# Performance work log

Hardware: AMD Instinct MI355X
Metric: run time of the kernel (lower is better)

## Reference

```python
import jax, jax.numpy as jnp
import numpy as np

B, S, D, H, HID = 8, 1024, 768, 12, 3072
HD = D // H
EPS = 1e-5


def layernorm(x, g, b):
    mu = jnp.mean(x, axis=-1, keepdims=True)
    var = jnp.mean(jnp.square(x - mu), axis=-1, keepdims=True)
    return (x - mu) * jax.lax.rsqrt(var + EPS) * g + b


def setup_inputs() -> dict:
    key = jax.random.key(0)
    ks = jax.random.split(key, 8)
    s_d = 1.0 / np.sqrt(D)
    s_h = 1.0 / np.sqrt(HID)
    return {
        "x": jax.random.normal(ks[0], (B, S, D), jnp.float32),
        # attention projections (stored as [in, out])
        "wq": jax.random.normal(ks[1], (D, D), jnp.float32) * s_d,
        "bq": jnp.zeros((D,), jnp.float32),
        "wk": jax.random.normal(ks[2], (D, D), jnp.float32) * s_d,
        "bk": jnp.zeros((D,), jnp.float32),
        "wv": jax.random.normal(ks[3], (D, D), jnp.float32) * s_d,
        "bv": jnp.zeros((D,), jnp.float32),
        # layernorms
        "ln1_g": jnp.ones((D,), jnp.float32),
        "ln1_b": jnp.zeros((D,), jnp.float32),
        "ln2_g": jnp.ones((D,), jnp.float32),
        "ln2_b": jnp.zeros((D,), jnp.float32),
        # MLP
        "w_in": jax.random.normal(ks[4], (D, HID), jnp.float32) * s_d,
        "b_in": jnp.zeros((HID,), jnp.float32),
        "w_out": jax.random.normal(ks[5], (HID, D), jnp.float32) * s_h,
        "b_out": jnp.zeros((D,), jnp.float32),
    }


def reference(x, wq, bq, wk, bk, wv, bv, ln1_g, ln1_b, ln2_g, ln2_b,
              w_in, b_in, w_out, b_out):
    scale = HD ** -0.5
    # --- MHSA (note: original forward never applies out_proj) ---
    q = (x @ wq + bq).reshape(B, S, H, HD).transpose(0, 2, 1, 3)  # [B,H,S,hd]
    k = (x @ wk + bk).reshape(B, S, H, HD).transpose(0, 2, 1, 3)
    v = (x @ wv + bv).reshape(B, S, H, HD).transpose(0, 2, 1, 3)
    scores = jnp.einsum("bhqd,bhkd->bhqk", q, k)  # full NxN, as in source
    attn = jax.nn.softmax(scores * scale, axis=-1)
    ctx = jnp.einsum("bhqk,bhkd->bhqd", attn, v)
    ctx = ctx.transpose(0, 2, 1, 3).reshape(B, S, D)
    # --- residual: pre_ln applied to attention OUTPUT (as in source) ---
    x = x + layernorm(ctx, ln1_g, ln1_b)
    # --- MLP: GELU after BOTH linears (as in source), dropout=0 ---
    h = jax.nn.gelu(layernorm(x, ln2_g, ln2_b) @ w_in + b_in, approximate=False)
    h = jax.nn.gelu(h @ w_out + b_out, approximate=False)
    return x + h
```

## Files before the change

### kernel.cpp

```cpp
#include <hip/hip_runtime.h>
#include <math.h>

typedef __attribute__((ext_vector_type(8))) short short8;
typedef __attribute__((ext_vector_type(4))) short short4v;
typedef __attribute__((ext_vector_type(4))) float f32x4;

#define MFMA16(a, b, c) __builtin_amdgcn_mfma_f32_16x16x32_bf16(a, b, c, 0, 0, 0)

__device__ __forceinline__ short f2bf(float f) {
    union { float f; unsigned u; } v; v.f = f;
    unsigned r = v.u + 0x7fffu + ((v.u >> 16) & 1u);
    return (short)(r >> 16);
}
__device__ __forceinline__ float bf2f(short s) {
    union { unsigned u; float f; } v; v.u = ((unsigned)(unsigned short)s) << 16;
    return v.f;
}
__device__ __forceinline__ float gelu(float v) {
    float u = v * (1.0f + 0.044715f * v * v);
    float e = exp2f(-2.3021184f * u);
    return v * __builtin_amdgcn_rcpf(1.0f + e);
}
__device__ __forceinline__ float max3f(float a, float b, float c) {
    float d; asm("v_max3_f32 %0, %1, %2, %3" : "=v"(d) : "v"(a), "v"(b), "v"(c)); return d;
}
__device__ __forceinline__ void async16(const short* g, short* l) {
    __builtin_amdgcn_global_load_lds((const __attribute__((address_space(1))) void*)g,
                                     (__attribute__((address_space(3))) void*)l, 16, 0, 0);
}

__device__ __forceinline__ short8 build_pfrag(int lg, float x0, float x1, float x2, float x3,
                                              float x4, float x5, float x6, float x7) {
    unsigned a0, a1, b0, b1;
    asm("v_cvt_pk_bf16_f32 %0, %1, %2" : "=v"(a0) : "v"(x0), "v"(x1));
    asm("v_cvt_pk_bf16_f32 %0, %1, %2" : "=v"(a1) : "v"(x2), "v"(x3));
    asm("v_cvt_pk_bf16_f32 %0, %1, %2" : "=v"(b0) : "v"(x4), "v"(x5));
    asm("v_cvt_pk_bf16_f32 %0, %1, %2" : "=v"(b1) : "v"(x6), "v"(x7));
    unsigned u0 = (lg < 2) ? b0 : a0, u1 = (lg < 2) ? b1 : a1;
    unsigned v0 = (unsigned)__shfl_xor((int)u0, 32), v1 = (unsigned)__shfl_xor((int)u1, 32);
    unsigned w0 = (lg < 2) ? a0 : b0, w1 = (lg < 2) ? a1 : b1;
    bool sw = ((lg ^ (lg >> 1)) & 1) != 0;
    unsigned s0 = sw ? w0 : v0, s1 = sw ? w1 : v1;
    unsigned r0 = (unsigned)__shfl_xor((int)s0, 16), r1 = (unsigned)__shfl_xor((int)s1, 16);
    union { unsigned u[4]; short8 s; } o;
    o.u[0] = (lg & 1) ? r0 : ((lg == 0) ? w0 : v0);
    o.u[1] = (lg & 1) ? r1 : ((lg == 0) ? w1 : v1);
    o.u[2] = (lg & 1) ? ((lg == 1) ? v0 : w0) : r0;
    o.u[3] = (lg & 1) ? ((lg == 1) ? v1 : w1) : r1;
    return o.s;
}

__global__ __launch_bounds__(256) void cast_kernel(const float* __restrict__ in,
                                                   short* __restrict__ out, int n4) {
    int i = blockIdx.x * 256 + threadIdx.x;
    if (i < n4) {
        float4 v = ((const float4*)in)[i];
        short4v o;
        o.x = f2bf(v.x); o.y = f2bf(v.y); o.z = f2bf(v.z); o.w = f2bf(v.w);
        ((short4v*)out)[i] = o;
    }
}

__global__ __launch_bounds__(256) void concat_bias(const float* __restrict__ a,
                                                   const float* __restrict__ b,
                                                   const float* __restrict__ c,
                                                   float* __restrict__ o) {
    int i = blockIdx.x * 256 + threadIdx.x;
    if (i < 768) o[i] = a[i];
    else if (i < 1536) o[i] = b[i - 768];
    else if (i < 2304) o[i] = c[i - 1536];
}

__global__ __launch_bounds__(256) void transpose_cast(const float* __restrict__ in,
                                                      short* __restrict__ out,
                                                      int K, int N) {
    __shared__ float tile[32][33];
    int n0 = blockIdx.x * 32, k0 = blockIdx.y * 32;
    int tx = threadIdx.x & 31, ty = threadIdx.x >> 5;
#pragma unroll
    for (int r = 0; r < 4; ++r)
        tile[ty + r * 8][tx] = in[(size_t)(k0 + ty + r * 8) * N + n0 + tx];
    __syncthreads();
#pragma unroll
    for (int r = 0; r < 4; ++r) {
        int rr = ty + r * 8;
        out[(size_t)(n0 + rr) * K + k0 + tx] = f2bf(tile[tx][rr]);
    }
}

__global__ __launch_bounds__(256) void transpose_v(const short* __restrict__ in,
                                                   short* __restrict__ out) {
    __shared__ short tile[32][33];
    const int bh = blockIdx.z;
    const int s0 = blockIdx.y * 32, d0 = blockIdx.x * 32;
    const short* src = in + (size_t)bh * 1024 * 64;
    short* dst = out + (size_t)bh * 64 * 1024;
    int tx = threadIdx.x & 31, ty = threadIdx.x >> 5;
#pragma unroll
    for (int r = 0; r < 4; ++r)
        tile[ty + r * 8][tx] = src[(size_t)(s0 + ty + r * 8) * 64 + d0 + tx];
    __syncthreads();
#pragma unroll
    for (int r = 0; r < 4; ++r) {
        int rr = ty + r * 8;
        dst[(size_t)(d0 + rr) * 1024 + s0 + tx] = tile[tx][rr];
    }
}

template <int EPI, int NF, int MB, int NXB>
__global__ __launch_bounds__(256) void gemm_kernel(const short* __restrict__ A,
                                                   const short* __restrict__ Bt,
                                                   const float* __restrict__ bias,
                                                   void* __restrict__ Cout,
                                                   const float* __restrict__ resid,
                                                   int M, int N, int K) {
    const int TN = NF * 32;
    const int FM = MB / 32;
    const int t = threadIdx.x;
    const int wid = t >> 6, lane = t & 63;
    const int wm = wid >> 1, wn = wid & 1;
    const int lr = lane & 15, lg = lane >> 4;

    const int wgid = blockIdx.x;
    const int xcd = wgid & 7;
    const int loc = wgid >> 3;
    const int rpx = (M / MB) >> 3;
    const int rb = xcd * rpx + loc / NXB;
    const int cb = loc % NXB;
    const int row0 = rb * MB, col0 = cb * TN;

    __shared__ __align__(16) short As[MB * 64];
    __shared__ __align__(16) short Bs[NF * 32 * 64];

    f32x4 acc[FM][NF];
#pragma unroll
    for (int i = 0; i < FM; ++i)
#pragma unroll
        for (int j = 0; j < NF; ++j) acc[i][j] = (f32x4){0.f, 0.f, 0.f, 0.f};

    const int aRow = wid * 8 + (lane >> 3);
    const int aK = ((lane & 7) ^ (lane >> 3)) << 3;
    const short* Ag = A + (size_t)(row0 + aRow) * K + aK;
    const short* Bg = Bt + (size_t)(col0 + aRow) * K + aK;
    short* AsW = As + wid * 8 * 64;
    short* BsW = Bs + wid * 8 * 64;
    const int swz = lr & 7;

    for (int k0 = 0; k0 < K; k0 += 64) {
        __syncthreads();
#pragma unroll
        for (int j = 0; j < MB / 32; ++j)
            async16(Ag + (size_t)(j * 32) * K + k0, AsW + j * 32 * 64);
#pragma unroll
        for (int j = 0; j < NF; ++j)
            async16(Bg + (size_t)(j * 32) * K + k0, BsW + j * 32 * 64);
        __syncthreads();

#pragma unroll
        for (int ks = 0; ks < 2; ++ks) {
            const int rdofs = ((ks * 4 + lg) ^ swz) << 3;
            short8 af[FM], bfr[NF];
#pragma unroll
            for (int i = 0; i < FM; ++i)
                af[i] = *(short8*)(As + (wm * (MB / 2) + i * 16 + lr) * 64 + rdofs);
#pragma unroll
            for (int i = 0; i < NF; ++i)
                bfr[i] = *(short8*)(Bs + (wn * (NF * 16) + i * 16 + lr) * 64 + rdofs);
#pragma unroll
            for (int mi = 0; mi < FM; ++mi)
#pragma unroll
                for (int ni = 0; ni < NF; ++ni)
                    acc[mi][ni] = MFMA16(af[mi], bfr[ni], acc[mi][ni]);
        }
    }

#pragma unroll
    for (int mi = 0; mi < FM; ++mi)
#pragma unroll
        for (int ni = 0; ni < NF; ++ni)
#pragma unroll
            for (int r = 0; r < 4; ++r) {
                int row = row0 + wm * (MB / 2) + mi * 16 + lg * 4 + r;
                int col = col0 + wn * (NF * 16) + ni * 16 + lr;
                float v = acc[mi][ni][r] + bias[col];
                if constexpr (EPI == 0) {
                    unsigned uc = (unsigned)col;
                    unsigned m = uc / 768u;
                    unsigned rest = uc - m * 768u;
                    unsigned h = rest >> 6, d = rest & 63u;
                    int b = row >> 10, s_ = row & 1023;
                    if (m == 0u) v *= 0.18033688011f;
                    ((short*)Cout)[((((size_t)m * 96 + (size_t)b * 12 + h) * 1024 + s_) * 64) + d] = f2bf(v);
                } else if constexpr (EPI == 1) {
                    ((short*)Cout)[(size_t)row * N + col] = f2bf(gelu(v));
                } else {
                    size_t idx = (size_t)row * N + col;
                    ((float*)Cout)[idx] = resid[idx] + gelu(v);
                }
            }
}

__global__ __launch_bounds__(256) void attn_kernel(const short* __restrict__ Q,
                                                   const short* __restrict__ Kg,
                                                   const short* __restrict__ VTg,
                                                   short* __restrict__ ctx) {
    const int bh = blockIdx.x;
    const int q0 = blockIdx.y * 64;
    const int t = threadIdx.x, wid = t >> 6, lane = t & 63;
    const int lr = lane & 15, lg = lane >> 4;

    __shared__ __align__(16) short Qs[64 * 64];
    __shared__ __align__(16) short Ks[64 * 64];
    __shared__ __align__(16) short Vt[64 * 64];

    const size_t base = (size_t)bh * 1024 * 64;
    const size_t vbase = (size_t)bh * 64 * 1024;

    const int srow = lane >> 3;
    const int lslot8 = ((lane & 7) ^ srow) << 3;
    const int r0w = wid * 16;
    const int swz = lr & 7;

    {
        const short* g = Q + base + (size_t)(q0 + r0w + srow) * 64 + lslot8;
        async16(g, Qs + r0w * 64);
        async16(g + 8 * 64, Qs + (r0w + 8) * 64);
    }
    __syncthreads();
    short8 qf[2];
    qf[0] = *(short8*)(Qs + (r0w + lr) * 64 + ((lg ^ swz) << 3));
    qf[1] = *(short8*)(Qs + (r0w + lr) * 64 + (((4 + lg) ^ swz) << 3));

    f32x4 oacc[4];
#pragma unroll
    for (int i = 0; i < 4; ++i) oacc[i] = (f32x4){0.f, 0.f, 0.f, 0.f};
    float mrun = -1e30f, lrun = 0.f;

    const short* kg = Kg + base + (size_t)(r0w + srow) * 64 + lslot8;
    const short* vg = VTg + vbase + (size_t)(r0w + srow) * 1024 + lslot8;

    for (int kt = 0; kt < 16; ++kt) {
        const int krow0 = kt * 64;
        __syncthreads();
        async16(kg + (size_t)krow0 * 64, Ks + r0w * 64);
        async16(kg + (size_t)(krow0 + 8) * 64, Ks + (r0w + 8) * 64);
        async16(vg + krow0, Vt + r0w * 64);
        async16(vg + krow0 + 8 * 1024, Vt + (r0w + 8) * 64);
        __syncthreads();

        f32x4 sfr[4];
#pragma unroll
        for (int cf = 0; cf < 4; ++cf) {
            f32x4 s = (f32x4){0.f, 0.f, 0.f, 0.f};
            short8 kf0 = *(short8*)(Ks + (cf * 16 + lr) * 64 + ((lg ^ swz) << 3));
            short8 kf1 = *(short8*)(Ks + (cf * 16 + lr) * 64 + (((4 + lg) ^ swz) << 3));
            s = MFMA16(kf0, qf[0], s);
            s = MFMA16(kf1, qf[1], s);
            sfr[cf] = s;
        }

        float g0 = max3f(sfr[0][0], sfr[0][1], sfr[0][2]);
        float g1 = max3f(sfr[0][3], sfr[1][0], sfr[1][1]);
        float g2 = max3f(sfr[1][2], sfr[1][3], sfr[2][0]);
        float g3 = max3f(sfr[2][1], sfr[2][2], sfr[2][3]);
        float g4 = max3f(sfr[3][0], sfr[3][1], sfr[3][2]);
        float mx = fmaxf(max3f(g0, g1, g2), max3f(g3, g4, sfr[3][3]));
        mx = fmaxf(mx, __shfl_xor(mx, 16));
        mx = fmaxf(mx, __shfl_xor(mx, 32));

        if (!__all(mx <= mrun + 8.0f)) {
            float mnew = fmaxf(mrun, mx);
            float fac = exp2f(mrun - mnew);
            lrun *= fac;
#pragma unroll
            for (int r = 0; r < 4; ++r) {
                float fr = __shfl(fac, lg * 4 + r);
#pragma unroll
                for (int df = 0; df < 4; ++df) oacc[df][r] *= fr;
            }
            mrun = mnew;
        }

        float p[16];
#pragma unroll
        for (int cf = 0; cf < 4; ++cf)
#pragma unroll
            for (int r = 0; r < 4; ++r) p[cf * 4 + r] = exp2f(sfr[cf][r] - mrun);
        float s0 = (p[0] + p[1]) + (p[2] + p[3]);
        float s1 = (p[4] + p[5]) + (p[6] + p[7]);
        float s2 = (p[8] + p[9]) + (p[10] + p[11]);
        float s3 = (p[12] + p[13]) + (p[14] + p[15]);
        float rs = (s0 + s1) + (s2 + s3);
        rs += __shfl_xor(rs, 16);
        rs += __shfl_xor(rs, 32);
        lrun += rs;

        short8 pf0 = build_pfrag(lg, p[0], p[1], p[2], p[3], p[4], p[5], p[6], p[7]);
        short8 pf1 = build_pfrag(lg, p[8], p[9], p[10], p[11], p[12], p[13], p[14], p[15]);
#pragma unroll
        for (int df = 0; df < 4; ++df) {
            short8 vf0 = *(short8*)(Vt + (df * 16 + lr) * 64 + ((lg ^ swz) << 3));
            oacc[df] = MFMA16(pf0, vf0, oacc[df]);
        }
#pragma unroll
        for (int df = 0; df < 4; ++df) {
            short8 vf1 = *(short8*)(Vt + (df * 16 + lr) * 64 + (((4 + lg) ^ swz) << 3));
            oacc[df] = MFMA16(pf1, vf1, oacc[df]);
        }
    }

    const int b = bh / 12, h = bh % 12;
    float rinv[4];
#pragma unroll
    for (int r = 0; r < 4; ++r) {
        float lr_ = __shfl(lrun, lg * 4 + r);
        rinv[r] = __builtin_amdgcn_rcpf(lr_);
    }
#pragma unroll
    for (int df = 0; df < 4; ++df)
#pragma unroll
        for (int r = 0; r < 4; ++r) {
            int q = q0 + wid * 16 + lg * 4 + r;
            int d = df * 16 + lr;
            float o = oacc[df][r] * rinv[r];
            ctx[((size_t)b * 1024 + q) * 768 + h * 64 + d] = f2bf(o);
        }
}

__global__ __launch_bounds__(256) void ln_fused(const float* __restrict__ x,
                                                const short* __restrict__ ctx,
                                                const float* __restrict__ g1,
                                                const float* __restrict__ b1,
                                                const float* __restrict__ g2,
                                                const float* __restrict__ b2,
                                                float* __restrict__ x2,
                                                short* __restrict__ ln2b) {
    const int row = blockIdx.x, t = threadIdx.x;
    const int wid = t >> 6, lane = t & 63;
    __shared__ float red[8];

    float c[3], xv[3];
#pragma unroll
    for (int j = 0; j < 3; ++j) {
        int idx = t + 256 * j;
        c[j] = bf2f(ctx[(size_t)row * 768 + idx]);
        xv[j] = x[(size_t)row * 768 + idx];
    }
    float s = c[0] + c[1] + c[2];
    float s2 = c[0] * c[0] + c[1] * c[1] + c[2] * c[2];
#pragma unroll
    for (int off = 32; off > 0; off >>= 1) { s += __shfl_down(s, off); s2 += __shfl_down(s2, off); }
    if (lane == 0) { red[wid] = s; red[4 + wid] = s2; }
    __syncthreads();
    s = red[0] + red[1] + red[2] + red[3];
    s2 = red[4] + red[5] + red[6] + red[7];
    float mu = s * (1.0f / 768.0f);
    float rstd = rsqrtf(s2 * (1.0f / 768.0f) - mu * mu + 1e-5f);

    float y[3];
#pragma unroll
    for (int j = 0; j < 3; ++j) {
        int idx = t + 256 * j;
        y[j] = xv[j] + (c[j] - mu) * rstd * g1[idx] + b1[idx];
        x2[(size_t)row * 768 + idx] = y[j];
    }
    __syncthreads();
    s = y[0] + y[1] + y[2];
    s2 = y[0] * y[0] + y[1] * y[1] + y[2] * y[2];
#pragma unroll
    for (int off = 32; off > 0; off >>= 1) { s += __shfl_down(s, off); s2 += __shfl_down(s2, off); }
    if (lane == 0) { red[wid] = s; red[4 + wid] = s2; }
    __syncthreads();
    s = red[0] + red[1] + red[2] + red[3];
    s2 = red[4] + red[5] + red[6] + red[7];
    float mu2 = s * (1.0f / 768.0f);
    float rstd2 = rsqrtf(s2 * (1.0f / 768.0f) - mu2 * mu2 + 1e-5f);
#pragma unroll
    for (int j = 0; j < 3; ++j) {
        int idx = t + 256 * j;
        ln2b[(size_t)row * 768 + idx] = f2bf((y[j] - mu2) * rstd2 * g2[idx] + b2[idx]);
    }
}

extern "C" void kernel_launch(void* const* d_in, const int* in_sizes, int n_in,
                              void* d_out, int out_size, void* d_ws, size_t ws_size,
                              hipStream_t stream) {
    const float* x    = (const float*)d_in[0];
    const float* wq   = (const float*)d_in[1];
    const float* bq   = (const float*)d_in[2];
    const float* wk   = (const float*)d_in[3];
    const float* bk   = (const float*)d_in[4];
    const float* wv   = (const float*)d_in[5];
    const float* bv   = (const float*)d_in[6];
    const float* g1   = (const float*)d_in[7];
    const float* b1   = (const float*)d_in[8];
    const float* g2   = (const float*)d_in[9];
    const float* b2   = (const float*)d_in[10];
    const float* w_in = (const float*)d_in[11];
    const float* b_in = (const float*)d_in[12];
    const float* w_out  = (const float*)d_in[13];
    const float* b_out  = (const float*)d_in[14];
    float* out = (float*)d_out;

    char* ws = (char*)d_ws;
    short* xb     = (short*)(ws + 0);
    short* vT     = (short*)(ws + 0);
    short* qb     = (short*)(ws + 12582912);
    short* kb     = (short*)(ws + 25165824);
    short* vb     = (short*)(ws + 37748736);
    short* h1     = (short*)(ws + 0);
    short* ctx    = (short*)(ws + 50331648);
    float* x2     = (float*)(ws + 62914560);
    float* bqkv   = (float*)(ws + 62914560);
    short* ln2b   = (short*)(ws + 88080384);
    short* wqkvT  = (short*)(ws + 100663296);
    short* w_inT  = (short*)(ws + 104202240);
    short* w_outT = (short*)(ws + 108920832);

    cast_kernel<<<6144, 256, 0, stream>>>(x, xb, 1572864);
    concat_bias<<<9, 256, 0, stream>>>(bq, bk, bv, bqkv);
    transpose_cast<<<dim3(24, 24), 256, 0, stream>>>(wq, wqkvT, 768, 768);
    transpose_cast<<<dim3(24, 24), 256, 0, stream>>>(wk, wqkvT + 768 * 768, 768, 768);
    transpose_cast<<<dim3(24, 24), 256, 0, stream>>>(wv, wqkvT + 2 * 768 * 768, 768, 768);
    transpose_cast<<<dim3(96, 24), 256, 0, stream>>>(w_in, w_inT, 768, 3072);
    transpose_cast<<<dim3(24, 96), 256, 0, stream>>>(w_out, w_outT, 3072, 768);

    gemm_kernel<0, 4, 128, 18><<<1152, 256, 0, stream>>>(xb, wqkvT, bqkv, qb, nullptr, 8192, 2304, 768);

    transpose_v<<<dim3(2, 32, 96), 256, 0, stream>>>(vb, vT);

    attn_kernel<<<dim3(96, 16), 256, 0, stream>>>(qb, kb, vT, ctx);

    ln_fused<<<8192, 256, 0, stream>>>(x, ctx, g1, b1, g2, b2, x2, ln2b);

    gemm_kernel<1, 4, 128, 24><<<1536, 256, 0, stream>>>(ln2b, w_inT, b_in, h1, nullptr, 8192, 3072, 768);
    gemm_kernel<2, 4, 64, 6><<<768, 256, 0, stream>>>(h1, w_outT, b_out, out, x2, 8192, 768, 3072);
}
```

Before: 372.3 us.

## Merge prep kernels, double attention query rows per warp, pack bf16 epilogue converts

Replaces the seven separate cast, bias-concat and weight-transpose launches with one prep kernel that picks its job from the block index, removing launch overhead. The attention kernel now handles 128 queries per block, with each warp holding two 16-row query groups. This reuses every K/V tile loaded into LDS twice as often and halves the grid, at the cost of more registers and fewer blocks. GEMM and attention epilogues convert pairs of values with the packed bf16 instruction and compute two rows per step. Q fragments are now read straight from global memory instead of being staged through LDS.

```diff
diff --git a/kernel.cpp b/kernel.cpp
--- a/kernel.cpp
+++ b/kernel.cpp
@@ -2,16 +2,14 @@
 #include <math.h>
 
 typedef __attribute__((ext_vector_type(8))) short short8;
-typedef __attribute__((ext_vector_type(4))) short short4v;
 typedef __attribute__((ext_vector_type(4))) float f32x4;
 
 #define MFMA16(a, b, c) __builtin_amdgcn_mfma_f32_16x16x32_bf16(a, b, c, 0, 0, 0)
 
-__device__ __forceinline__ short f2bf(float f) {
-    union { float f; unsigned u; } v; v.f = f;
-    unsigned r = v.u + 0x7fffu + ((v.u >> 16) & 1u);
-    return (short)(r >> 16);
-}
+__device__ __forceinline__ unsigned cvtpk(float a, float b) {
+    unsigned r; asm("v_cvt_pk_bf16_f32 %0, %1, %2" : "=v"(r) : "v"(a), "v"(b)); return r;
+}
+__device__ __forceinline__ short f2bf(float f) { return (short)cvtpk(f, f); }
 __device__ __forceinline__ float bf2f(short s) {
     union { unsigned u; float f; } v; v.u = ((unsigned)(unsigned short)s) << 16;
     return v.f;
@@ -31,11 +29,8 @@
 
 __device__ __forceinline__ short8 build_pfrag(int lg, float x0, float x1, float x2, float x3,
                                               float x4, float x5, float x6, float x7) {
-    unsigned a0, a1, b0, b1;
-    asm("v_cvt_pk_bf16_f32 %0, %1, %2" : "=v"(a0) : "v"(x0), "v"(x1));
-    asm("v_cvt_pk_bf16_f32 %0, %1, %2" : "=v"(a1) : "v"(x2), "v"(x3));
-    asm("v_cvt_pk_bf16_f32 %0, %1, %2" : "=v"(b0) : "v"(x4), "v"(x5));
-    asm("v_cvt_pk_bf16_f32 %0, %1, %2" : "=v"(b1) : "v"(x6), "v"(x7));
+    unsigned a0 = cvtpk(x0, x1), a1 = cvtpk(x2, x3);
+    unsigned b0 = cvtpk(x4, x5), b1 = cvtpk(x6, x7);
     unsigned u0 = (lg < 2) ? b0 : a0, u1 = (lg < 2) ? b1 : a1;
     unsigned v0 = (unsigned)__shfl_xor((int)u0, 32), v1 = (unsigned)__shfl_xor((int)u1, 32);
     unsigned w0 = (lg < 2) ? a0 : b0, w1 = (lg < 2) ? a1 : b1;
@@ -50,33 +45,46 @@
     return o.s;
 }
 
-__global__ __launch_bounds__(256) void cast_kernel(const float* __restrict__ in,
-                                                   short* __restrict__ out, int n4) {
-    int i = blockIdx.x * 256 + threadIdx.x;
-    if (i < n4) {
-        float4 v = ((const float4*)in)[i];
-        short4v o;
-        o.x = f2bf(v.x); o.y = f2bf(v.y); o.z = f2bf(v.z); o.w = f2bf(v.w);
-        ((short4v*)out)[i] = o;
-    }
-}
-
-__global__ __launch_bounds__(256) void concat_bias(const float* __restrict__ a,
-                                                   const float* __restrict__ b,
-                                                   const float* __restrict__ c,
-                                                   float* __restrict__ o) {
-    int i = blockIdx.x * 256 + threadIdx.x;
-    if (i < 768) o[i] = a[i];
-    else if (i < 1536) o[i] = b[i - 768];
-    else if (i < 2304) o[i] = c[i - 1536];
-}
-
-__global__ __launch_bounds__(256) void transpose_cast(const float* __restrict__ in,
-                                                      short* __restrict__ out,
-                                                      int K, int N) {
+__global__ __launch_bounds__(256) void prep_kernel(
+    const float* __restrict__ x, short* __restrict__ xb,
+    const float* __restrict__ bq, const float* __restrict__ bk,
+    const float* __restrict__ bv, float* __restrict__ bqkv,
+    const float* __restrict__ wq, const float* __restrict__ wk,
+    const float* __restrict__ wv, short* __restrict__ wqkvT,
+    const float* __restrict__ w_in, short* __restrict__ w_inT,
+    const float* __restrict__ w_out, short* __restrict__ w_outT) {
     __shared__ float tile[32][33];
-    int n0 = blockIdx.x * 32, k0 = blockIdx.y * 32;
-    int tx = threadIdx.x & 31, ty = threadIdx.x >> 5;
+    const int w = blockIdx.x, t = threadIdx.x;
+    if (w < 6144) {
+        int i = w * 256 + t;
+        float4 v = ((const float4*)x)[i];
+        uint2 o; o.x = cvtpk(v.x, v.y); o.y = cvtpk(v.z, v.w);
+        ((uint2*)xb)[i] = o;
+        return;
+    }
+    if (w < 6153) {
+        int i = (w - 6144) * 256 + t;
+        if (i < 768) bqkv[i] = bq[i];
+        else if (i < 1536) bqkv[i] = bk[i - 768];
+        else if (i < 2304) bqkv[i] = bv[i - 1536];
+        return;
+    }
+    const float* in; short* out; int K, N, n0, k0;
+    if (w < 7881) {
+        int v_ = w - 6153, z = v_ / 576, u = v_ - z * 576;
+        in = (z == 0) ? wq : (z == 1) ? wk : wv;
+        out = wqkvT + (size_t)z * 768 * 768;
+        K = 768; N = 768; n0 = (u % 24) * 32; k0 = (u / 24) * 32;
+    } else if (w < 10185) {
+        int u = w - 7881;
+        in = w_in; out = w_inT; K = 768; N = 3072;
+        n0 = (u % 96) * 32; k0 = (u / 96) * 32;
+    } else {
+        int u = w - 10185;
+        in = w_out; out = w_outT; K = 3072; N = 768;
+        n0 = (u % 24) * 32; k0 = (u / 24) * 32;
+    }
+    int tx = t & 31, ty = t >> 5;
 #pragma unroll
     for (int r = 0; r < 4; ++r)
         tile[ty + r * 8][tx] = in[(size_t)(k0 + ty + r * 8) * N + n0 + tx];
@@ -179,23 +187,31 @@
 #pragma unroll
         for (int ni = 0; ni < NF; ++ni)
 #pragma unroll
-            for (int r = 0; r < 4; ++r) {
-                int row = row0 + wm * (MB / 2) + mi * 16 + lg * 4 + r;
+            for (int rp = 0; rp < 4; rp += 2) {
+                int row = row0 + wm * (MB / 2) + mi * 16 + lg * 4 + rp;
                 int col = col0 + wn * (NF * 16) + ni * 16 + lr;
-                float v = acc[mi][ni][r] + bias[col];
+                float v0 = acc[mi][ni][rp] + bias[col];
+                float v1 = acc[mi][ni][rp + 1] + bias[col];
                 if constexpr (EPI == 0) {
                     unsigned uc = (unsigned)col;
                     unsigned m = uc / 768u;
                     unsigned rest = uc - m * 768u;
                     unsigned h = rest >> 6, d = rest & 63u;
                     int b = row >> 10, s_ = row & 1023;
-                    if (m == 0u) v *= 0.18033688011f;
-                    ((short*)Cout)[((((size_t)m * 96 + (size_t)b * 12 + h) * 1024 + s_) * 64) + d] = f2bf(v);
+                    if (m == 0u) { v0 *= 0.18033688011f; v1 *= 0.18033688011f; }
+                    unsigned pk = cvtpk(v0, v1);
+                    size_t idx = ((((size_t)m * 96 + (size_t)b * 12 + h) * 1024 + s_) * 64) + d;
+                    ((short*)Cout)[idx] = (short)pk;
+                    ((short*)Cout)[idx + 64] = (short)(pk >> 16);
                 } else if constexpr (EPI == 1) {
-                    ((short*)Cout)[(size_t)row * N + col] = f2bf(gelu(v));
+                    unsigned pk = cvtpk(gelu(v0), gelu(v1));
+                    size_t idx = (size_t)row * N + col;
+                    ((short*)Cout)[idx] = (short)pk;
+                    ((short*)Cout)[idx + N] = (short)(pk >> 16);
                 } else {
                     size_t idx = (size_t)row * N + col;
-                    ((float*)Cout)[idx] = resid[idx] + gelu(v);
+                    ((float*)Cout)[idx] = resid[idx] + gelu(v0);
+                    ((float*)Cout)[idx + N] = resid[idx + N] + gelu(v1);
                 }
             }
 }
@@ -205,11 +221,10 @@
                                                    const short* __restrict__ VTg,
                                                    short* __restrict__ ctx) {
     const int bh = blockIdx.x;
-    const int q0 = blockIdx.y * 64;
+    const int q0 = blockIdx.y * 128;
     const int t = threadIdx.x, wid = t >> 6, lane = t & 63;
     const int lr = lane & 15, lg = lane >> 4;
 
-    __shared__ __align__(16) short Qs[64 * 64];
     __shared__ __align__(16) short Ks[64 * 64];
     __shared__ __align__(16) short Vt[64 * 64];
 
@@ -221,20 +236,21 @@
     const int r0w = wid * 16;
     const int swz = lr & 7;
 
+    short8 qf[2][2];
     {
-        const short* g = Q + base + (size_t)(q0 + r0w + srow) * 64 + lslot8;
-        async16(g, Qs + r0w * 64);
-        async16(g + 8 * 64, Qs + (r0w + 8) * 64);
-    }
-    __syncthreads();
-    short8 qf[2];
-    qf[0] = *(short8*)(Qs + (r0w + lr) * 64 + ((lg ^ swz) << 3));
-    qf[1] = *(short8*)(Qs + (r0w + lr) * 64 + (((4 + lg) ^ swz) << 3));
-
-    f32x4 oacc[4];
-#pragma unroll
-    for (int i = 0; i < 4; ++i) oacc[i] = (f32x4){0.f, 0.f, 0.f, 0.f};
-    float mrun = -1e30f, lrun = 0.f;
+        const short* qrow = Q + base + (size_t)(q0 + wid * 32 + lr) * 64;
+        qf[0][0] = *(const short8*)(qrow + lg * 8);
+        qf[0][1] = *(const short8*)(qrow + 32 + lg * 8);
+        qf[1][0] = *(const short8*)(qrow + 16 * 64 + lg * 8);
+        qf[1][1] = *(const short8*)(qrow + 16 * 64 + 32 + lg * 8);
+    }
+
+    f32x4 oacc[2][4];
+#pragma unroll
+    for (int g = 0; g < 2; ++g)
+#pragma unroll
+        for (int i = 0; i < 4; ++i) oacc[g][i] = (f32x4){0.f, 0.f, 0.f, 0.f};
+    float mrun[2] = {-1e30f, -1e30f}, lrun[2] = {0.f, 0.f};
 
     const short* kg = Kg + base + (size_t)(r0w + srow) * 64 + lslot8;
     const short* vg = VTg + vbase + (size_t)(r0w + srow) * 1024 + lslot8;
@@ -248,83 +264,99 @@
         async16(vg + krow0 + 8 * 1024, Vt + (r0w + 8) * 64);
         __syncthreads();
 
-        f32x4 sfr[4];
+        f32x4 sfr[2][4];
 #pragma unroll
         for (int cf = 0; cf < 4; ++cf) {
-            f32x4 s = (f32x4){0.f, 0.f, 0.f, 0.f};
             short8 kf0 = *(short8*)(Ks + (cf * 16 + lr) * 64 + ((lg ^ swz) << 3));
             short8 kf1 = *(short8*)(Ks + (cf * 16 + lr) * 64 + (((4 + lg) ^ swz) << 3));
-            s = MFMA16(kf0, qf[0], s);
-            s = MFMA16(kf1, qf[1], s);
-            sfr[cf] = s;
-        }
-
-        float g0 = max3f(sfr[0][0], sfr[0][1], sfr[0][2]);
-        float g1 = max3f(sfr[0][3], sfr[1][0], sfr[1][1]);
-        float g2 = max3f(sfr[1][2], sfr[1][3], sfr[2][0]);
-        float g3 = max3f(sfr[2][1], sfr[2][2], sfr[2][3]);
-        float g4 = max3f(sfr[3][0], sfr[3][1], sfr[3][2]);
-        float mx = fmaxf(max3f(g0, g1, g2), max3f(g3, g4, sfr[3][3]));
-        mx = fmaxf(mx, __shfl_xor(mx, 16));
-        mx = fmaxf(mx, __shfl_xor(mx, 32));
-
-        if (!__all(mx <= mrun + 8.0f)) {
-            float mnew = fmaxf(mrun, mx);
-            float fac = exp2f(mrun - mnew);
-            lrun *= fac;
-#pragma unroll
-            for (int r = 0; r < 4; ++r) {
-                float fr = __shfl(fac, lg * 4 + r);
-#pragma unroll
-                for (int df = 0; df < 4; ++df) oacc[df][r] *= fr;
+#pragma unroll
+            for (int g = 0; g < 2; ++g) {
+                f32x4 s = (f32x4){0.f, 0.f, 0.f, 0.f};
+                s = MFMA16(kf0, qf[g][0], s);
+                s = MFMA16(kf1, qf[g][1], s);
+                sfr[g][cf] = s;
             }
-            mrun = mnew;
-        }
-
-        float p[16];
-#pragma unroll
-        for (int cf = 0; cf < 4; ++cf)
-#pragma unroll
-            for (int r = 0; r < 4; ++r) p[cf * 4 + r] = exp2f(sfr[cf][r] - mrun);
-        float s0 = (p[0] + p[1]) + (p[2] + p[3]);
-        float s1 = (p[4] + p[5]) + (p[6] + p[7]);
-        float s2 = (p[8] + p[9]) + (p[10] + p[11]);
-        float s3 = (p[12] + p[13]) + (p[14] + p[15]);
-        float rs = (s0 + s1) + (s2 + s3);
-        rs += __shfl_xor(rs, 16);
-        rs += __shfl_xor(rs, 32);
-        lrun += rs;
-
-        short8 pf0 = build_pfrag(lg, p[0], p[1], p[2], p[3], p[4], p[5], p[6], p[7]);
-        short8 pf1 = build_pfrag(lg, p[8], p[9], p[10], p[11], p[12], p[13], p[14], p[15]);
+        }
+
+        short8 pf[2][2];
+#pragma unroll
+        for (int g = 0; g < 2; ++g) {
+            float g0 = max3f(sfr[g][0][0], sfr[g][0][1], sfr[g][0][2]);
+            float g1 = max3f(sfr[g][0][3], sfr[g][1][0], sfr[g][1][1]);
+            float g2 = max3f(sfr[g][1][2], sfr[g][1][3], sfr[g][2][0]);
+            float g3 = max3f(sfr[g][2][1], sfr[g][2][2], sfr[g][2][3]);
+            float g4 = max3f(sfr[g][3][0], sfr[g][3][1], sfr[g][3][2]);
+            float mx = fmaxf(max3f(g0, g1, g2), max3f(g3, g4, sfr[g][3][3]));
+            mx = fmaxf(mx, __shfl_xor(mx, 16));
+            mx = fmaxf(mx, __shfl_xor(mx, 32));
+
+            if (!__all(mx <= mrun[g] + 8.0f)) {
+                float mnew = fmaxf(mrun[g], mx);
+                float fac = exp2f(mrun[g] - mnew);
+                lrun[g] *= fac;
+#pragma unroll
+                for (int r = 0; r < 4; ++r) {
+                    float fr = __shfl(fac, lg * 4 + r);
+#pragma unroll
+                    for (int df = 0; df < 4; ++df) oacc[g][df][r] *= fr;
+                }
+                mrun[g] = mnew;
+            }
+
+            float p[16];
+#pragma unroll
+            for (int cf = 0; cf < 4; ++cf)
+#pragma unroll
+                for (int r = 0; r < 4; ++r) p[cf * 4 + r] = exp2f(sfr[g][cf][r] - mrun[g]);
+            float s0 = (p[0] + p[1]) + (p[2] + p[3]);
+            float s1 = (p[4] + p[5]) + (p[6] + p[7]);
+            float s2 = (p[8] + p[9]) + (p[10] + p[11]);
+            float s3 = (p[12] + p[13]) + (p[14] + p[15]);
+            float rs = (s0 + s1) + (s2 + s3);
+            rs += __shfl_xor(rs, 16);
+            rs += __shfl_xor(rs, 32);
+            lrun[g] += rs;
+
+            pf[g][0] = build_pfrag(lg, p[0], p[1], p[2], p[3], p[4], p[5], p[6], p[7]);
+            pf[g][1] = build_pfrag(lg, p[8], p[9], p[10], p[11], p[12], p[13], p[14], p[15]);
+        }
+
 #pragma unroll
         for (int df = 0; df < 4; ++df) {
             short8 vf0 = *(short8*)(Vt + (df * 16 + lr) * 64 + ((lg ^ swz) << 3));
-            oacc[df] = MFMA16(pf0, vf0, oacc[df]);
+            oacc[0][df] = MFMA16(pf[0][0], vf0, oacc[0][df]);
+            oacc[1][df] = MFMA16(pf[1][0], vf0, oacc[1][df]);
         }
 #pragma unroll
         for (int df = 0; df < 4; ++df) {
             short8 vf1 = *(short8*)(Vt + (df * 16 + lr) * 64 + (((4 + lg) ^ swz) << 3));
-            oacc[df] = MFMA16(pf1, vf1, oacc[df]);
+            oacc[0][df] = MFMA16(pf[0][1], vf1, oacc[0][df]);
+            oacc[1][df] = MFMA16(pf[1][1], vf1, oacc[1][df]);
         }
     }
 
     const int b = bh / 12, h = bh % 12;
-    float rinv[4];
-#pragma unroll
-    for (int r = 0; r < 4; ++r) {
-        float lr_ = __shfl(lrun, lg * 4 + r);
-        rinv[r] = __builtin_amdgcn_rcpf(lr_);
-    }
-#pragma unroll
-    for (int df = 0; df < 4; ++df)
+#pragma unroll
+    for (int g = 0; g < 2; ++g) {
+        float rinv[4];
 #pragma unroll
         for (int r = 0; r < 4; ++r) {
-            int q = q0 + wid * 16 + lg * 4 + r;
-            int d = df * 16 + lr;
-            float o = oacc[df][r] * rinv[r];
-            ctx[((size_t)b * 1024 + q) * 768 + h * 64 + d] = f2bf(o);
-        }
+            float lr_ = __shfl(lrun[g], lg * 4 + r);
+            rinv[r] = __builtin_amdgcn_rcpf(lr_);
+        }
+#pragma unroll
+        for (int df = 0; df < 4; ++df)
+#pragma unroll
+            for (int rp = 0; rp < 4; rp += 2) {
+                int q = q0 + wid * 32 + g * 16 + lg * 4 + rp;
+                int d = df * 16 + lr;
+                unsigned pk = cvtpk(oacc[g][df][rp] * rinv[rp],
+                                    oacc[g][df][rp + 1] * rinv[rp + 1]);
+                size_t idx = ((size_t)b * 1024 + q) * 768 + h * 64 + d;
+                ctx[idx] = (short)pk;
+                ctx[idx + 768] = (short)(pk >> 16);
+            }
+    }
 }
 
 __global__ __launch_bounds__(256) void ln_fused(const float* __restrict__ x,
@@ -417,19 +449,14 @@
     short* w_inT  = (short*)(ws + 104202240);
     short* w_outT = (short*)(ws + 108920832);
 
-    cast_kernel<<<6144, 256, 0, stream>>>(x, xb, 1572864);
-    concat_bias<<<9, 256, 0, stream>>>(bq, bk, bv, bqkv);
-    transpose_cast<<<dim3(24, 24), 256, 0, stream>>>(wq, wqkvT, 768, 768);
-    transpose_cast<<<dim3(24, 24), 256, 0, stream>>>(wk, wqkvT + 768 * 768, 768, 768);
-    transpose_cast<<<dim3(24, 24), 256, 0, stream>>>(wv, wqkvT + 2 * 768 * 768, 768, 768);
-    transpose_cast<<<dim3(96, 24), 256, 0, stream>>>(w_in, w_inT, 768, 3072);
-    transpose_cast<<<dim3(24, 96), 256, 0, stream>>>(w_out, w_outT, 3072, 768);
+    prep_kernel<<<12489, 256, 0, stream>>>(x, xb, bq, bk, bv, bqkv,
+                                           wq, wk, wv, wqkvT, w_in, w_inT, w_out, w_outT);
 
     gemm_kernel<0, 4, 128, 18><<<1152, 256, 0, stream>>>(xb, wqkvT, bqkv, qb, nullptr, 8192, 2304, 768);
 
     transpose_v<<<dim3(2, 32, 96), 256, 0, stream>>>(vb, vT);
 
-    attn_kernel<<<dim3(96, 16), 256, 0, stream>>>(qb, kb, vT, ctx);
+    attn_kernel<<<dim3(96, 8), 256, 0, stream>>>(qb, kb, vT, ctx);
 
     ln_fused<<<8192, 256, 0, stream>>>(x, ctx, g1, b1, g2, b2, x2, ln2b);
 
```

Result: faster. 348.5 us (-6.4%).
